# Optimization experiments

Measured on AMD Instinct MI355X. Metric: run time of the kernel, lower is better.

Reference implementation:

```python
import jax, jax.numpy as jnp
import numpy as np

B, S, HID = 2, 2048, 2048
NH, NKV, D = 32, 8, 64
G = NH // NKV
THETA = 150000.0


def rotate_half(x):
    x1, x2 = x[..., : D // 2], x[..., D // 2 :]
    return jnp.concatenate([-x2, x1], axis=-1)


def setup_inputs() -> dict:
    key = jax.random.key(0)
    ks = jax.random.split(key, 10)
    sc = 0.02
    return {
        "hidden_states": jax.random.normal(ks[0], (B, S, HID), jnp.float32),
        "position_ids": jnp.arange(S, dtype=jnp.int64 if jax.config.jax_enable_x64 else jnp.int32),
        "wq": jax.random.normal(ks[1], (HID, NH * D), jnp.float32) * sc,
        "bq": jax.random.normal(ks[2], (NH * D,), jnp.float32) * sc,
        "wk": jax.random.normal(ks[3], (HID, NKV * D), jnp.float32) * sc,
        "bk": jax.random.normal(ks[4], (NKV * D,), jnp.float32) * sc,
        "wv": jax.random.normal(ks[5], (HID, NKV * D), jnp.float32) * sc,
        "bv": jax.random.normal(ks[6], (NKV * D,), jnp.float32) * sc,
        "wo": jax.random.normal(ks[7], (NH * D, HID), jnp.float32) * sc,
        "bo": jax.random.normal(ks[8], (HID,), jnp.float32) * sc,
    }


def reference(hidden_states, position_ids, wq, bq, wk, bk, wv, bv, wo, bo):
    # projections: [B,S,NH,D] / [B,S,NKV,D] -> head-major
    q = (hidden_states @ wq + bq).reshape(B, S, NH, D).transpose(0, 2, 1, 3)   # [B,NH,S,D]
    k = (hidden_states @ wk + bk).reshape(B, S, NKV, D).transpose(0, 2, 1, 3)  # [B,NKV,S,D]
    v = (hidden_states @ wv + bv).reshape(B, S, NKV, D).transpose(0, 2, 1, 3)

    # HF RoPE: inv_freq over even dims, freqs duplicated across the two halves
    inv_freq = 1.0 / (THETA ** (jnp.arange(0, D, 2, dtype=jnp.float32) / D))   # [D/2]
    freqs = position_ids.astype(jnp.float32)[:, None] * inv_freq[None, :]      # [S,D/2]
    emb = jnp.concatenate([freqs, freqs], axis=-1)                             # [S,D]
    cos = jnp.cos(emb)[None, None]  # [1,1,S,D]
    sin = jnp.sin(emb)[None, None]
    q = q * cos + rotate_half(q) * sin
    k = k * cos + rotate_half(k) * sin

    # GQA: group query heads by kv head instead of repeat_interleave on K/V
    qg = q.reshape(B, NKV, G, S, D)
    scores = jnp.einsum("bkgsd,bktd->bkgst", qg, k) / jnp.sqrt(jnp.float32(D))  # [B,NKV,G,S,S]
    attn = jax.nn.softmax(scores, axis=-1)
    out = jnp.einsum("bkgst,bktd->bkgsd", attn, v)                              # [B,NKV,G,S,D]
    out = out.reshape(B, NH, S, D).transpose(0, 2, 1, 3).reshape(B, S, NH * D)  # [B,S,NH*D]
    return out @ wo + bo
```

## Files before the change

### kernel.cpp

```cpp
#include <hip/hip_runtime.h>
#include <hip/hip_bf16.h>
#include <math.h>

#define B_   2
#define S_   2048
#define HID_ 2048
#define NH_  32
#define NKV_ 8
#define D_   64
#define G_   (NH_/NKV_)
#define M_   (B_*S_)

typedef __hip_bfloat16 bf16;
typedef short bf16x8 __attribute__((ext_vector_type(8)));
typedef float f32x4  __attribute__((ext_vector_type(4)));
typedef unsigned short u16x4 __attribute__((ext_vector_type(4)));

__device__ inline unsigned short f2bfu(float f){
    __hip_bfloat16 h = __float2bfloat16(f);
    return __builtin_bit_cast(unsigned short, h);
}

__device__ __forceinline__ float fexp2(float x){
#if __has_builtin(__builtin_amdgcn_exp2f)
    return __builtin_amdgcn_exp2f(x);
#else
    return exp2f(x);
#endif
}

__device__ __forceinline__ void async16(const void* g, void* l) {
    __builtin_amdgcn_global_load_lds(
        (const __attribute__((address_space(1))) unsigned int*)g,
        (__attribute__((address_space(3))) unsigned int*)l, 16, 0, 0);
}

#define SWZ(r, c) ((c) ^ (((r) & 7) << 3))

__global__ __launch_bounds__(256) void cvt_k(
    const float* __restrict__ src, bf16* __restrict__ dst, int n)
{
    const int i = (blockIdx.x * 256 + threadIdx.x) * 8;
    if (i >= n) return;
    const float4 a = *(const float4*)(src + i);
    const float4 b = *(const float4*)(src + i + 4);
    uint4 u;
    u.x = (unsigned)f2bfu(a.x) | ((unsigned)f2bfu(a.y) << 16);
    u.y = (unsigned)f2bfu(a.z) | ((unsigned)f2bfu(a.w) << 16);
    u.z = (unsigned)f2bfu(b.x) | ((unsigned)f2bfu(b.y) << 16);
    u.w = (unsigned)f2bfu(b.z) | ((unsigned)f2bfu(b.w) << 16);
    *(uint4*)((unsigned short*)dst + i) = u;
}

__global__ __launch_bounds__(256) void wtrans_k(
    const float* __restrict__ s0, int N0,
    const float* __restrict__ s1, int N1,
    const float* __restrict__ s2, int N2,
    bf16* __restrict__ dst, int K)
{
    __shared__ unsigned short t[64][65];
    const int ntile = blockIdx.x * 64, ktile = blockIdx.y * 64;
    const float* src; int nloc, Nseg;
    if (ntile < N0)           { src = s0; nloc = ntile;           Nseg = N0; }
    else if (ntile < N0 + N1) { src = s1; nloc = ntile - N0;      Nseg = N1; }
    else                      { src = s2; nloc = ntile - N0 - N1; Nseg = N2; }
    const int r  = threadIdx.x >> 4;
    const int c4 = (threadIdx.x & 15) * 4;
    #pragma unroll
    for (int p = 0; p < 4; p++) {
        const int k = p * 16 + r;
        const float4 f = *(const float4*)(src + (size_t)(ktile + k) * Nseg + nloc + c4);
        t[k][c4+0] = f2bfu(f.x); t[k][c4+1] = f2bfu(f.y);
        t[k][c4+2] = f2bfu(f.z); t[k][c4+3] = f2bfu(f.w);
    }
    __syncthreads();
    #pragma unroll
    for (int p = 0; p < 4; p++) {
        const int n = p * 16 + r;
        u16x4 u = { t[c4+0][n], t[c4+1][n], t[c4+2][n], t[c4+3][n] };
        *(u16x4*)((unsigned short*)dst + (size_t)(ntile + n) * K + ktile + c4) = u;
    }
}

__global__ __launch_bounds__(256) void rope_tab_k(
    const int* __restrict__ pos, float* __restrict__ ctab, float* __restrict__ stab)
{
    const int idx = blockIdx.x * 256 + threadIdx.x;
    if (idx >= S_ * 32) return;
    const int s = idx >> 5, i = idx & 31;
    const int is64 = (pos[1] == 0);
    const int p = is64 ? pos[2 * s] : pos[s];
    const double inv = exp(-(double)i * (log(150000.0) / 32.0));
    const double f = (double)p * inv;
    ctab[idx] = (float)cos(f);
    stab[idx] = (float)sin(f);
}

template<int MODE>
__global__ __launch_bounds__(256) void gemm128_k(
    const bf16* __restrict__ A, const bf16* __restrict__ WT,
    const float* __restrict__ b0, const float* __restrict__ b1,
    const float* __restrict__ b2,
    bf16* __restrict__ Cq, bf16* __restrict__ Ck, bf16* __restrict__ Cv,
    float* __restrict__ Cout,
    const float* __restrict__ ctab, const float* __restrict__ stab)
{
    __shared__ unsigned short sA[128 * 64];
    __shared__ unsigned short sB[128 * 64];

    const int tid  = threadIdx.x;
    const int wave = tid >> 6, lane = tid & 63;
    const int li   = lane & 15, lj = lane >> 4;
    const int m0   = blockIdx.y * 128;
    const int n0   = blockIdx.x * 128;
    const int wm   = (wave >> 1) * 64, wn = (wave & 1) * 64;
    const int K    = 2048;

    f32x4 acc[4][4];
    #pragma unroll
    for (int i = 0; i < 4; i++)
        #pragma unroll
        for (int j = 0; j < 4; j++)
            acc[i][j] = (f32x4){0.f, 0.f, 0.f, 0.f};

    const bf16* ag = A  + (size_t)(m0 + wave * 32 + (lane >> 3)) * K + (lane & 7) * 8;
    const bf16* bg = WT + (size_t)(n0 + wave * 32 + (lane >> 3)) * K + (lane & 7) * 8;
    unsigned short* la = &sA[(wave * 32) * 64];
    unsigned short* lb = &sB[(wave * 32) * 64];

    for (int k0 = 0; k0 < K; k0 += 64) {
        __syncthreads();
        #pragma unroll
        for (int i = 0; i < 4; i++) {
            async16(ag + k0 + (size_t)i * 8 * K, la + i * 8 * 64);
            async16(bg + k0 + (size_t)i * 8 * K, lb + i * 8 * 64);
        }
        __syncthreads();

        #pragma unroll
        for (int ks = 0; ks < 64; ks += 32) {
            bf16x8 af[4], bfr[4];
            #pragma unroll
            for (int mt = 0; mt < 4; mt++)
                af[mt] = *(const bf16x8*)&sA[(wm + mt * 16 + li) * 64 + ks + lj * 8];
            #pragma unroll
            for (int nt = 0; nt < 4; nt++)
                bfr[nt] = *(const bf16x8*)&sB[(wn + nt * 16 + li) * 64 + ks + lj * 8];
            #pragma unroll
            for (int mt = 0; mt < 4; mt++)
                #pragma unroll
                for (int nt = 0; nt < 4; nt++)
                    acc[mt][nt] = __builtin_amdgcn_mfma_f32_16x16x32_bf16(
                        af[mt], bfr[nt], acc[mt][nt], 0, 0, 0);
        }
    }

    if (MODE == 1) {
        #pragma unroll
        for (int mt = 0; mt < 4; mt++)
            #pragma unroll
            for (int nt = 0; nt < 4; nt++) {
                const int col = n0 + wn + nt * 16 + li;
                const float bb = b0[col];
                #pragma unroll
                for (int r = 0; r < 4; r++) {
                    const int row = m0 + wm + mt * 16 + lj * 4 + r;
                    Cout[(size_t)row * HID_ + col] = acc[mt][nt][r] + bb;
                }
            }
        return;
    }

    int seg, cb; const float* bias;
    if (n0 < 2048)      { seg = 0; cb = n0;        bias = b0; }
    else if (n0 < 2560) { seg = 1; cb = n0 - 2048; bias = b1; }
    else                { seg = 2; cb = n0 - 2560; bias = b2; }

    float bl[4];
    #pragma unroll
    for (int nt = 0; nt < 4; nt++) bl[nt] = bias[cb + wn + nt * 16 + li];

    if (seg == 2) {
        const int b = m0 >> 11;
        #pragma unroll
        for (int nt = 0; nt < 4; nt++) {
            const int cseg = cb + wn + nt * 16 + li;
            const int hv = cseg >> 6, d = cseg & 63;
            #pragma unroll
            for (int mt = 0; mt < 4; mt++) {
                const int sb = (m0 & (S_ - 1)) + wm + mt * 16 + lj * 4;
                u16x4 u = { f2bfu(acc[mt][nt][0] + bl[nt]),
                            f2bfu(acc[mt][nt][1] + bl[nt]),
                            f2bfu(acc[mt][nt][2] + bl[nt]),
                            f2bfu(acc[mt][nt][3] + bl[nt]) };
                *(u16x4*)((unsigned short*)Cv +
                    ((size_t)((b * NKV_ + hv) * 64 + d)) * S_ + sb) = u;
            }
        }
        return;
    }

    const float qs = (seg == 0) ? 0.18033688011112042f : 1.0f;
    #pragma unroll
    for (int mt = 0; mt < 4; mt++) {
        #pragma unroll
        for (int r = 0; r < 4; r++) {
            const int row = m0 + wm + mt * 16 + lj * 4 + r;
            const int s = row & (S_ - 1);
            const float c0  = ctab[s * 32 + li],      sn0 = stab[s * 32 + li];
            const float c1  = ctab[s * 32 + 16 + li], sn1 = stab[s * 32 + 16 + li];
            const float x0 = acc[mt][0][r] + bl[0];
            const float x1 = acc[mt][1][r] + bl[1];
            const float x2 = acc[mt][2][r] + bl[2];
            const float x3 = acc[mt][3][r] + bl[3];
            const float y0 = (x0 * c0 - x2 * sn0) * qs;
            const float y2 = (x2 * c0 + x0 * sn0) * qs;
            const float y1 = (x1 * c1 - x3 * sn1) * qs;
            const float y3 = (x3 * c1 + x1 * sn1) * qs;
            if (seg == 0) {
                bf16* cp = Cq + (size_t)row * HID_ + n0 + wn + li;
                cp[0]  = __float2bfloat16(y0);
                cp[16] = __float2bfloat16(y1);
                cp[32] = __float2bfloat16(y2);
                cp[48] = __float2bfloat16(y3);
            } else {
                bf16* cp = Ck + (size_t)row * 512 + cb + wn + li;
                cp[0]  = __float2bfloat16(y0);
                cp[16] = __float2bfloat16(y1);
                cp[32] = __float2bfloat16(y2);
                cp[48] = __float2bfloat16(y3);
            }
        }
    }
}

__global__ __launch_bounds__(256, 4) void attn_k(
    const bf16* __restrict__ qws, const bf16* __restrict__ kws,
    const bf16* __restrict__ vtw, bf16* __restrict__ ows)
{
    __shared__ unsigned short sK [64 * 64];
    __shared__ unsigned short sVt[64 * 64];
    __shared__ unsigned short sP [4 * 32 * 64];

    const int tid  = threadIdx.x;
    const int wave = tid >> 6, lane = tid & 63;
    const int li   = lane & 15, lj = lane >> 4;
    const int bh   = blockIdx.y;
    const int q0   = blockIdx.x * 128;
    const int b    = bh / NH_, h = bh % NH_;
    const int hk   = h / G_;

    bf16x8 qf[2][2];
    #pragma unroll
    for (int g = 0; g < 2; g++) {
        const bf16* qp = qws + (size_t)(b * S_ + q0 + wave * 32 + g * 16 + li) * HID_
                         + h * D_ + lj * 8;
        qf[g][0] = *(const bf16x8*)(qp);
        qf[g][1] = *(const bf16x8*)(qp + 32);
    }

    f32x4 o[2][4];
    #pragma unroll
    for (int g = 0; g < 2; g++)
        #pragma unroll
        for (int mt = 0; mt < 4; mt++) o[g][mt] = (f32x4){0.f, 0.f, 0.f, 0.f};
    float mr[2] = {-1e30f, -1e30f};
    float ll[2] = {0.f, 0.f};

    const int srow = tid >> 2, scol = (tid & 3) * 16;
    const bf16* kb = kws + (size_t)b * S_ * 512 + hk * 64;
    const bf16* vb = vtw + (size_t)((b * NKV_ + hk) * 64) * S_;
    unsigned short* sp = sP + wave * (32 * 64);

    uint4 pk0, pk1, pv0, pv1;
    {
        const uint4* kp = (const uint4*)(kb + (size_t)srow * 512 + scol);
        const uint4* vp = (const uint4*)(vb + (size_t)srow * S_ + scol);
        pk0 = kp[0]; pk1 = kp[1]; pv0 = vp[0]; pv1 = vp[1];
    }

    for (int kt = 0; kt < S_; kt += 64) {
        __syncthreads();
        *(uint4*)&sK [srow * 64 + SWZ(srow, scol)]     = pk0;
        *(uint4*)&sK [srow * 64 + SWZ(srow, scol + 8)] = pk1;
        *(uint4*)&sVt[srow * 64 + SWZ(srow, scol)]     = pv0;
        *(uint4*)&sVt[srow * 64 + SWZ(srow, scol + 8)] = pv1;
        __syncthreads();

        if (kt + 64 < S_) {
            const uint4* kp = (const uint4*)(kb + (size_t)(kt + 64 + srow) * 512 + scol);
            const uint4* vp = (const uint4*)(vb + (size_t)srow * S_ + kt + 64 + scol);
            pk0 = kp[0]; pk1 = kp[1]; pv0 = vp[0]; pv1 = vp[1];
        }

        float sc[2][4][4];
        __builtin_amdgcn_s_setprio(1);
        #pragma unroll
        for (int nt = 0; nt < 4; nt++) {
            f32x4 c0 = (f32x4){0.f, 0.f, 0.f, 0.f};
            f32x4 c1 = (f32x4){0.f, 0.f, 0.f, 0.f};
            #pragma unroll
            for (int ks = 0; ks < 2; ks++) {
                const bf16x8 kf =
                    *(const bf16x8*)&sK[(nt * 16 + li) * 64 + SWZ(li, ks * 32 + lj * 8)];
                c0 = __builtin_amdgcn_mfma_f32_16x16x32_bf16(kf, qf[0][ks], c0, 0, 0, 0);
                c1 = __builtin_amdgcn_mfma_f32_16x16x32_bf16(kf, qf[1][ks], c1, 0, 0, 0);
            }
            #pragma unroll
            for (int r = 0; r < 4; r++) { sc[0][nt][r] = c0[r]; sc[1][nt][r] = c1[r]; }
        }
        __builtin_amdgcn_s_setprio(0);

        #pragma unroll
        for (int g = 0; g < 2; g++) {
            float cm = sc[g][0][0];
            #pragma unroll
            for (int nt = 0; nt < 4; nt++)
                #pragma unroll
                for (int r = 0; r < 4; r++) cm = fmaxf(cm, sc[g][nt][r]);
            cm = fmaxf(cm, __shfl_xor(cm, 16));
            cm = fmaxf(cm, __shfl_xor(cm, 32));
            if (!__all(cm - mr[g] <= 8.0f)) {
                const float mnew = fmaxf(mr[g], cm);
                const float al   = fexp2(mr[g] - mnew);
                mr[g] = mnew;
                ll[g] *= al;
                #pragma unroll
                for (int mt = 0; mt < 4; mt++) o[g][mt] *= al;
            }
            float rs = 0.f;
            #pragma unroll
            for (int nt = 0; nt < 4; nt++) {
                const float e0 = fexp2(sc[g][nt][0] - mr[g]);
                const float e1 = fexp2(sc[g][nt][1] - mr[g]);
                const float e2 = fexp2(sc[g][nt][2] - mr[g]);
                const float e3 = fexp2(sc[g][nt][3] - mr[g]);
                rs += (e0 + e1) + (e2 + e3);
                u16x4 u = { f2bfu(e0), f2bfu(e1), f2bfu(e2), f2bfu(e3) };
                *(u16x4*)&sp[(g * 16 + li) * 64 + SWZ(li, nt * 16 + lj * 4)] = u;
            }
            ll[g] += rs;
        }

        __builtin_amdgcn_s_setprio(1);
        #pragma unroll
        for (int ks = 0; ks < 2; ks++) {
            const bf16x8 pf0 = *(const bf16x8*)&sp[(li)      * 64 + SWZ(li, ks * 32 + lj * 8)];
            const bf16x8 pf1 = *(const bf16x8*)&sp[(16 + li) * 64 + SWZ(li, ks * 32 + lj * 8)];
            #pragma unroll
            for (int mt = 0; mt < 4; mt++) {
                const bf16x8 vf =
                    *(const bf16x8*)&sVt[(mt * 16 + li) * 64 + SWZ(li, ks * 32 + lj * 8)];
                o[0][mt] = __builtin_amdgcn_mfma_f32_16x16x32_bf16(vf, pf0, o[0][mt], 0, 0, 0);
                o[1][mt] = __builtin_amdgcn_mfma_f32_16x16x32_bf16(vf, pf1, o[1][mt], 0, 0, 0);
            }
        }
        __builtin_amdgcn_s_setprio(0);
    }

    #pragma unroll
    for (int g = 0; g < 2; g++) {
        float l = ll[g];
        l += __shfl_xor(l, 16);
        l += __shfl_xor(l, 32);
        const float inv = 1.0f / l;
        bf16* op = ows + (size_t)(b * S_ + q0 + wave * 32 + g * 16 + li) * HID_ + h * D_;
        #pragma unroll
        for (int mt = 0; mt < 4; mt++) {
            u16x4 u = { f2bfu(o[g][mt][0] * inv), f2bfu(o[g][mt][1] * inv),
                        f2bfu(o[g][mt][2] * inv), f2bfu(o[g][mt][3] * inv) };
            *(u16x4*)((unsigned short*)op + mt * 16 + lj * 4) = u;
        }
    }
}

extern "C" void kernel_launch(void* const* d_in, const int* in_sizes, int n_in,
                              void* d_out, int out_size, void* d_ws, size_t ws_size,
                              hipStream_t stream)
{
    const float* hs  = (const float*)d_in[0];
    const int*   pos = (const int*)d_in[1];
    const float* wq = (const float*)d_in[2];
    const float* bq = (const float*)d_in[3];
    const float* wk = (const float*)d_in[4];
    const float* bk = (const float*)d_in[5];
    const float* wv = (const float*)d_in[6];
    const float* bv = (const float*)d_in[7];
    const float* wo = (const float*)d_in[8];
    const float* bo = (const float*)d_in[9];

    char* ws = (char*)d_ws;
    float* ctab  = (float*)(ws);
    float* stab  = (float*)(ws + (256u << 10));
    bf16*  k_ws  = (bf16*)(ws + (512u << 10));
    bf16*  v_t   = (bf16*)(ws + (512u << 10) + (4u  << 20));
    bf16*  q_ws  = (bf16*)(ws + (512u << 10) + (8u  << 20));
    bf16*  woT   = q_ws;
    bf16*  hs_b  = (bf16*)(ws + (512u << 10) + (24u << 20));
    bf16*  o_ws  = hs_b;
    bf16*  wqkvT = (bf16*)(ws + (512u << 10) + (40u << 20));

    rope_tab_k<<<dim3(256), dim3(256), 0, stream>>>(pos, ctab, stab);

    cvt_k<<<dim3(M_ * HID_ / 2048), dim3(256), 0, stream>>>(hs, hs_b, M_ * HID_);

    wtrans_k<<<dim3(48, 32), dim3(256), 0, stream>>>(
        wq, 2048, wk, 512, wv, 512, wqkvT, HID_);

    gemm128_k<0><<<dim3(24, 32), dim3(256), 0, stream>>>(
        hs_b, wqkvT, bq, bk, bv, q_ws, k_ws, v_t, nullptr, ctab, stab);

    attn_k<<<dim3(S_ / 128, B_ * NH_), dim3(256), 0, stream>>>(q_ws, k_ws, v_t, o_ws);

    wtrans_k<<<dim3(32, 32), dim3(256), 0, stream>>>(
        wo, 2048, wo, 0, wo, 0, woT, HID_);

    gemm128_k<1><<<dim3(16, 32), dim3(256), 0, stream>>>(
        o_ws, woT, bo, nullptr, nullptr, nullptr, nullptr, nullptr,
        (float*)d_out, nullptr, nullptr);
}
```

Measured before the change: 371.4 us.

## Replace GEMM kernel with 256-wide double-buffered, LDS-swizzled, 8-wave MFMA pipeline

Replaces the 128x128 single-buffered GEMM with a 512-thread kernel using 256-wide N tiles (256 or 128 M) and two LDS buffers. Global-to-LDS async loads for tile t+2 are issued while tile t is computed, with explicit vmcnt waits and raw barriers. The LDS layout is XOR-swizzled to avoid bank conflicts, and A-fragment loads are software-pipelined with setprio around MFMA bursts. The larger tiles and explicit wait counts add LDS pressure (up to 128KB) and fewer blocks per grid, which risks lower occupancy or tail imbalance.

New measurement: 347.4 us. -6.5%, faster.

```diff
diff --git a/kernel.cpp b/kernel.cpp
--- a/kernel.cpp
+++ b/kernel.cpp
@@ -36,6 +36,11 @@
 }
 
 #define SWZ(r, c) ((c) ^ (((r) & 7) << 3))
+
+#define S_BARRIER() asm volatile("s_barrier" ::: "memory")
+__device__ __forceinline__ void vmwait8(){ asm volatile("s_waitcnt vmcnt(8)" ::: "memory"); }
+__device__ __forceinline__ void vmwait6(){ asm volatile("s_waitcnt vmcnt(6)" ::: "memory"); }
+__device__ __forceinline__ void vmwait0(){ asm volatile("s_waitcnt vmcnt(0)" ::: "memory"); }
 
 __global__ __launch_bounds__(256) void cvt_k(
     const float* __restrict__ src, bf16* __restrict__ dst, int n)
@@ -96,8 +101,74 @@
     stab[idx] = (float)sin(f);
 }
 
-template<int MODE>
-__global__ __launch_bounds__(256) void gemm128_k(
+
+template<int BM>
+__device__ __forceinline__ void stage_g(
+    const bf16* __restrict__ A, const bf16* __restrict__ B,
+    int m0, int n0, int k0,
+    unsigned short* sAb, unsigned short* sBb, int wave, int lane)
+{
+    const int rr = wave * 8 + (lane >> 3);
+    const int cc = ((lane & 7) ^ (lane >> 3)) * 8;
+    #pragma unroll
+    for (int i = 0; i < BM / 64; ++i)
+        async16(A + (size_t)(m0 + i * 64 + rr) * 2048 + k0 + cc,
+                sAb + i * 4096 + wave * 512);
+    #pragma unroll
+    for (int j = 0; j < 4; ++j)
+        async16(B + (size_t)(n0 + j * 64 + rr) * 2048 + k0 + cc,
+                sBb + j * 4096 + wave * 512);
+}
+
+template<int BM>
+__device__ __forceinline__ void tile_mfma(
+    const unsigned short* sAb, const unsigned short* sBb,
+    int wm, int wn, int li, int lj, f32x4 (*acc)[4])
+{
+    constexpr int MT = BM / 32;
+    constexpr int PM = MT / 4;
+    const int swz = li & 7;
+
+    bf16x8 bfr[4][2];
+    #pragma unroll
+    for (int nt = 0; nt < 4; ++nt)
+        #pragma unroll
+        for (int ks = 0; ks < 2; ++ks)
+            bfr[nt][ks] = *(const bf16x8*)
+                &sBb[(wn * 64 + nt * 16 + li) * 64 + ((ks * 4 + lj) ^ swz) * 8];
+
+    bf16x8 afA[PM][2], afB[PM][2];
+    auto lda = [&](bf16x8 (*dst)[2], int p) {
+        #pragma unroll
+        for (int m = 0; m < PM; ++m)
+            #pragma unroll
+            for (int ks = 0; ks < 2; ++ks)
+                dst[m][ks] = *(const bf16x8*)
+                    &sAb[(wm * (BM / 2) + (p * PM + m) * 16 + li) * 64
+                         + ((ks * 4 + lj) ^ swz) * 8];
+    };
+    lda(afA, 0);
+    #pragma unroll
+    for (int p = 0; p < 4; ++p) {
+        bf16x8 (*cur)[2] = (p & 1) ? afB : afA;
+        bf16x8 (*nxt)[2] = (p & 1) ? afA : afB;
+        if (p < 3) lda(nxt, p + 1);
+        __builtin_amdgcn_s_setprio(1);
+        #pragma unroll
+        for (int ks = 0; ks < 2; ++ks)
+            #pragma unroll
+            for (int m = 0; m < PM; ++m)
+                #pragma unroll
+                for (int nt = 0; nt < 4; ++nt)
+                    acc[p * PM + m][nt] = __builtin_amdgcn_mfma_f32_16x16x32_bf16(
+                        cur[m][ks], bfr[nt][ks], acc[p * PM + m][nt], 0, 0, 0);
+        __builtin_amdgcn_s_setprio(0);
+        __builtin_amdgcn_sched_barrier(0);
+    }
+}
+
+template<int MODE, int BM>
+__global__ __launch_bounds__(512, 2) void gemm256_k(
     const bf16* __restrict__ A, const bf16* __restrict__ WT,
     const float* __restrict__ b0, const float* __restrict__ b1,
     const float* __restrict__ b2,
@@ -105,66 +176,56 @@
     float* __restrict__ Cout,
     const float* __restrict__ ctab, const float* __restrict__ stab)
 {
-    __shared__ unsigned short sA[128 * 64];
-    __shared__ unsigned short sB[128 * 64];
+    constexpr int MT = BM / 32;
+    constexpr int LA = BM * 64;
+    constexpr int LB = 256 * 64;
+    constexpr int NT = 2048 / 64;
+    __shared__ unsigned short sA[2 * LA];
+    __shared__ unsigned short sB[2 * LB];
 
     const int tid  = threadIdx.x;
     const int wave = tid >> 6, lane = tid & 63;
     const int li   = lane & 15, lj = lane >> 4;
-    const int m0   = blockIdx.y * 128;
-    const int n0   = blockIdx.x * 128;
-    const int wm   = (wave >> 1) * 64, wn = (wave & 1) * 64;
-    const int K    = 2048;
-
-    f32x4 acc[4][4];
-    #pragma unroll
-    for (int i = 0; i < 4; i++)
-        #pragma unroll
-        for (int j = 0; j < 4; j++)
+    const int wm   = wave >> 2, wn = wave & 3;
+    const int m0   = blockIdx.y * BM;
+    const int n0   = blockIdx.x * 256;
+
+    f32x4 acc[MT][4];
+    #pragma unroll
+    for (int i = 0; i < MT; ++i)
+        #pragma unroll
+        for (int j = 0; j < 4; ++j)
             acc[i][j] = (f32x4){0.f, 0.f, 0.f, 0.f};
 
-    const bf16* ag = A  + (size_t)(m0 + wave * 32 + (lane >> 3)) * K + (lane & 7) * 8;
-    const bf16* bg = WT + (size_t)(n0 + wave * 32 + (lane >> 3)) * K + (lane & 7) * 8;
-    unsigned short* la = &sA[(wave * 32) * 64];
-    unsigned short* lb = &sB[(wave * 32) * 64];
-
-    for (int k0 = 0; k0 < K; k0 += 64) {
-        __syncthreads();
-        #pragma unroll
-        for (int i = 0; i < 4; i++) {
-            async16(ag + k0 + (size_t)i * 8 * K, la + i * 8 * 64);
-            async16(bg + k0 + (size_t)i * 8 * K, lb + i * 8 * 64);
-        }
-        __syncthreads();
-
-        #pragma unroll
-        for (int ks = 0; ks < 64; ks += 32) {
-            bf16x8 af[4], bfr[4];
-            #pragma unroll
-            for (int mt = 0; mt < 4; mt++)
-                af[mt] = *(const bf16x8*)&sA[(wm + mt * 16 + li) * 64 + ks + lj * 8];
-            #pragma unroll
-            for (int nt = 0; nt < 4; nt++)
-                bfr[nt] = *(const bf16x8*)&sB[(wn + nt * 16 + li) * 64 + ks + lj * 8];
-            #pragma unroll
-            for (int mt = 0; mt < 4; mt++)
-                #pragma unroll
-                for (int nt = 0; nt < 4; nt++)
-                    acc[mt][nt] = __builtin_amdgcn_mfma_f32_16x16x32_bf16(
-                        af[mt], bfr[nt], acc[mt][nt], 0, 0, 0);
-        }
+    stage_g<BM>(A, WT, m0, n0, 0,  sA,      sB,      wave, lane);
+    stage_g<BM>(A, WT, m0, n0, 64, sA + LA, sB + LB, wave, lane);
+    if constexpr (BM == 256) vmwait8(); else vmwait6();
+    S_BARRIER();
+
+    for (int t = 0; t < NT; ++t) {
+        const int buf = t & 1;
+        tile_mfma<BM>(sA + buf * LA, sB + buf * LB, wm, wn, li, lj, acc);
+        S_BARRIER();
+        if (t + 2 < NT) {
+            stage_g<BM>(A, WT, m0, n0, (t + 2) * 64,
+                        sA + buf * LA, sB + buf * LB, wave, lane);
+            if constexpr (BM == 256) vmwait8(); else vmwait6();
+        } else {
+            vmwait0();
+        }
+        S_BARRIER();
     }
 
     if (MODE == 1) {
         #pragma unroll
-        for (int mt = 0; mt < 4; mt++)
-            #pragma unroll
-            for (int nt = 0; nt < 4; nt++) {
-                const int col = n0 + wn + nt * 16 + li;
+        for (int mt = 0; mt < MT; ++mt)
+            #pragma unroll
+            for (int nt = 0; nt < 4; ++nt) {
+                const int col = n0 + wn * 64 + nt * 16 + li;
                 const float bb = b0[col];
                 #pragma unroll
-                for (int r = 0; r < 4; r++) {
-                    const int row = m0 + wm + mt * 16 + lj * 4 + r;
+                for (int r = 0; r < 4; ++r) {
+                    const int row = m0 + wm * (BM / 2) + mt * 16 + lj * 4 + r;
                     Cout[(size_t)row * HID_ + col] = acc[mt][nt][r] + bb;
                 }
             }
@@ -178,17 +239,17 @@
 
     float bl[4];
     #pragma unroll
-    for (int nt = 0; nt < 4; nt++) bl[nt] = bias[cb + wn + nt * 16 + li];
+    for (int nt = 0; nt < 4; ++nt) bl[nt] = bias[cb + wn * 64 + nt * 16 + li];
 
     if (seg == 2) {
         const int b = m0 >> 11;
         #pragma unroll
-        for (int nt = 0; nt < 4; nt++) {
-            const int cseg = cb + wn + nt * 16 + li;
+        for (int nt = 0; nt < 4; ++nt) {
+            const int cseg = cb + wn * 64 + nt * 16 + li;
             const int hv = cseg >> 6, d = cseg & 63;
             #pragma unroll
-            for (int mt = 0; mt < 4; mt++) {
-                const int sb = (m0 & (S_ - 1)) + wm + mt * 16 + lj * 4;
+            for (int mt = 0; mt < MT; ++mt) {
+                const int sb = (m0 & (S_ - 1)) + wm * (BM / 2) + mt * 16 + lj * 4;
                 u16x4 u = { f2bfu(acc[mt][nt][0] + bl[nt]),
                             f2bfu(acc[mt][nt][1] + bl[nt]),
                             f2bfu(acc[mt][nt][2] + bl[nt]),
@@ -202,10 +263,10 @@
 
     const float qs = (seg == 0) ? 0.18033688011112042f : 1.0f;
     #pragma unroll
-    for (int mt = 0; mt < 4; mt++) {
-        #pragma unroll
-        for (int r = 0; r < 4; r++) {
-            const int row = m0 + wm + mt * 16 + lj * 4 + r;
+    for (int mt = 0; mt < MT; ++mt) {
+        #pragma unroll
+        for (int r = 0; r < 4; ++r) {
+            const int row = m0 + wm * (BM / 2) + mt * 16 + lj * 4 + r;
             const int s = row & (S_ - 1);
             const float c0  = ctab[s * 32 + li],      sn0 = stab[s * 32 + li];
             const float c1  = ctab[s * 32 + 16 + li], sn1 = stab[s * 32 + 16 + li];
@@ -218,13 +279,13 @@
             const float y1 = (x1 * c1 - x3 * sn1) * qs;
             const float y3 = (x3 * c1 + x1 * sn1) * qs;
             if (seg == 0) {
-                bf16* cp = Cq + (size_t)row * HID_ + n0 + wn + li;
+                bf16* cp = Cq + (size_t)row * HID_ + n0 + wn * 64 + li;
                 cp[0]  = __float2bfloat16(y0);
                 cp[16] = __float2bfloat16(y1);
                 cp[32] = __float2bfloat16(y2);
                 cp[48] = __float2bfloat16(y3);
             } else {
-                bf16* cp = Ck + (size_t)row * 512 + cb + wn + li;
+                bf16* cp = Ck + (size_t)row * 512 + cb + wn * 64 + li;
                 cp[0]  = __float2bfloat16(y0);
                 cp[16] = __float2bfloat16(y1);
                 cp[32] = __float2bfloat16(y2);
@@ -407,7 +468,7 @@
     wtrans_k<<<dim3(48, 32), dim3(256), 0, stream>>>(
         wq, 2048, wk, 512, wv, 512, wqkvT, HID_);
 
-    gemm128_k<0><<<dim3(24, 32), dim3(256), 0, stream>>>(
+    gemm256_k<0, 256><<<dim3(12, 16), dim3(512), 0, stream>>>(
         hs_b, wqkvT, bq, bk, bv, q_ws, k_ws, v_t, nullptr, ctab, stab);
 
     attn_k<<<dim3(S_ / 128, B_ * NH_), dim3(256), 0, stream>>>(q_ws, k_ws, v_t, o_ws);
@@ -415,7 +476,7 @@
     wtrans_k<<<dim3(32, 32), dim3(256), 0, stream>>>(
         wo, 2048, wo, 0, wo, 0, woT, HID_);
 
-    gemm128_k<1><<<dim3(16, 32), dim3(256), 0, stream>>>(
+    gemm256_k<1, 128><<<dim3(8, 32), dim3(512), 0, stream>>>(
         o_ws, woT, bo, nullptr, nullptr, nullptr, nullptr, nullptr,
         (float*)d_out, nullptr, nullptr);
 }
```
